# Kernel tuning notes

Measured on AMD Instinct MI355X. Metric: run time of the kernel, lower is better.

## Reference

```python
import jax, jax.numpy as jnp
import numpy as np

SINKHORN_ITERS = 10


def _optimal_transport(attn, phi, iters):
    # attn: [N,H,W,W], phi: scalar dustbin score
    bs, h, w, _ = attn.shape
    marginal = jnp.concatenate([jnp.ones((w,), attn.dtype), jnp.array([float(w)], attn.dtype)]) / (2.0 * w)
    log_mu = jnp.log(marginal)  # [W+1], broadcasts over [N,H,W+1]
    log_nu = log_mu
    # augment with dustbin row/col filled with phi -> [N,H,W+1,W+1]
    sim = jnp.concatenate([attn, jnp.broadcast_to(phi, (bs, h, w, 1))], axis=-1)
    sim = jnp.concatenate([sim, jnp.broadcast_to(phi, (bs, h, 1, w + 1))], axis=-2)

    def body(i, uv):
        u, v = uv
        v = log_nu - jax.nn.logsumexp(sim + u[..., :, None], axis=2)
        u = log_mu - jax.nn.logsumexp(sim + v[..., None, :], axis=3)
        return (u, v)

    u0 = jnp.zeros((bs, h, w + 1), attn.dtype)
    u, v = jax.lax.fori_loop(0, iters, body, (u0, u0))
    attn_ot = sim + u[..., :, None] + v[..., None, :]
    return jnp.exp(attn_ot + jnp.log(2.0 * w))


def _compute_low_res_disp(pos_shift, attn, occ_mask=None):
    # attn: [N,H,W,W] (dustbins removed); pos_shift: [W,W]
    w = attn.shape[-1]
    high_response = jnp.argmax(attn, axis=-1)  # [N,H,W]
    response_range = jnp.stack([high_response - 1, high_response, high_response + 1], axis=-1)  # [N,H,W,3]
    attn_pad = jnp.pad(attn, ((0, 0), (0, 0), (0, 0), (1, 1)))
    attn_rw = jnp.take_along_axis(attn_pad, response_range + 1, axis=-1)  # [N,H,W,3]
    norm = attn_rw.sum(-1, keepdims=True)
    norm = jnp.where(norm < 0.1, 1.0, norm)  # occ_mask is None branch
    attn_rw = attn_rw / norm
    pos_pad = jnp.pad(pos_shift, ((0, 0), (1, 1)))  # [W,W+2]
    pos_pad = jnp.broadcast_to(pos_pad[None, None], attn_pad.shape)
    pos_rw = jnp.take_along_axis(pos_pad, response_range + 1, axis=-1)
    disp = (attn_rw * pos_rw).sum(-1)  # [N,H,W]
    return disp, norm


def setup_inputs() -> dict:
    key = jax.random.key(0)
    k1, _ = jax.random.split(key)
    N, H, W = 4, 120, 256
    attn_weight = jax.random.normal(k1, (N, H, W, W), dtype=jnp.float32)
    phi = jnp.zeros((1,), dtype=jnp.float32)
    return {"attn_weight": attn_weight, "phi": phi}


def reference(attn_weight, phi):
    w = attn_weight.shape[2]
    attn_ot = _optimal_transport(attn_weight, phi[0], SINKHORN_ITERS)  # [N,H,W+1,W+1]
    # relative position shift, clamped at 0
    pos = jnp.arange(w, dtype=attn_weight.dtype)
    pos_shift = jnp.maximum(pos[:, None] - pos[None, :], 0.0)  # [W,W]
    disp_pred_low_res, matched_attn = _compute_low_res_disp(pos_shift, attn_ot[..., :-1, :-1], None)
    occ_pred = 1.0 - matched_attn.squeeze(-1)  # [N,H,W]
    return disp_pred_low_res, occ_pred
```

## Files before the change

### kernel.cpp

```cpp
#include <hip/hip_runtime.h>
#include <cstdint>

namespace {

constexpr int W = 256;
constexpr int ITERS = 10;
constexpr int PSTR = 260;

__device__ __forceinline__ float dpp_add_xor1(float x) {
  int y = __builtin_amdgcn_mov_dpp(__float_as_int(x), 0xB1, 0xF, 0xF, true);
  return x + __int_as_float(y);
}
__device__ __forceinline__ float dpp_add_xor2(float x) {
  int y = __builtin_amdgcn_mov_dpp(__float_as_int(x), 0x4E, 0xF, 0xF, true);
  return x + __int_as_float(y);
}
template <int PAT>
__device__ __forceinline__ float swz_add(float x) {
  return x + __int_as_float(__builtin_amdgcn_ds_swizzle(__float_as_int(x), PAT));
}
__device__ __forceinline__ float allred32(float x) {
  x = dpp_add_xor1(x);
  x = dpp_add_xor2(x);
  x = swz_add<0x101F>(x);
  x = swz_add<0x201F>(x);
  x = swz_add<0x401F>(x);
  return x;
}
__device__ __forceinline__ float rcpf(float x) {
  float r;
  asm("v_rcp_f32 %0, %1" : "=v"(r) : "v"(x));
  return r;
}

__global__ __launch_bounds__(1024)
void sinkhorn_disp_kernel(
    const float* __restrict__ attn,
    const float* __restrict__ phi_p,
    float* __restrict__ out,
    int nh)
{
  __shared__ __align__(16) float E_lds[1024 * 32];
  __shared__ __align__(16) float fpart[16][PSTR];
  __shared__ __align__(16) float ev_l[W];
  __shared__ __align__(16) float seup[32];
  __shared__ float evW_s;

  const int tid = threadIdx.x;
  const int tc  = tid & 31;
  const int tr  = tid >> 5;
  const int bid = blockIdx.x;
  const int sw  = tid & 7;
  float* myE = &E_lds[tid * 32];
  #define RDCH(c) (*(const float4*)&myE[4 * ((c) ^ sw)])

  const float ephi  = __int_as_float(
      __builtin_amdgcn_readfirstlane(__float_as_int(__expf(phi_p[0]))));
  const float inv2w = 1.0f / (2.0f * W);

  const int ch0 = 4 * ((2 * tc) ^ ((tc >> 2) & 7));

  float Er[5][8];
  {
    const float* src = attn + (size_t)bid * (W * W) + (size_t)(tr * 8) * W + tc * 8;
    #pragma unroll
    for (int a = 0; a < 5; ++a) {
      float4 x0 = *(const float4*)(src + a * W);
      float4 x1 = *(const float4*)(src + a * W + 4);
      Er[a][0] = __expf(x0.x); Er[a][1] = __expf(x0.y);
      Er[a][2] = __expf(x0.z); Er[a][3] = __expf(x0.w);
      Er[a][4] = __expf(x1.x); Er[a][5] = __expf(x1.y);
      Er[a][6] = __expf(x1.z); Er[a][7] = __expf(x1.w);
    }
    #pragma unroll
    for (int r = 0; r < 3; ++r) {
      float4 x0 = *(const float4*)(src + (5 + r) * W);
      float4 x1 = *(const float4*)(src + (5 + r) * W + 4);
      *(float4*)&myE[4 * ((2 + 2 * r) ^ sw)] =
          make_float4(__expf(x0.x), __expf(x0.y), __expf(x0.z), __expf(x0.w));
      *(float4*)&myE[4 * ((3 + 2 * r) ^ sw)] =
          make_float4(__expf(x1.x), __expf(x1.y), __expf(x1.z), __expf(x1.w));
    }
  }

  float eul[8];
  #pragma unroll
  for (int a = 0; a < 8; ++a) eul[a] = 1.0f;
  float euW = 1.0f;

  for (int it = 0; it < ITERS; ++it) {
    if (it >= 2 && it <= 5 && bid + 256 < nh) {
      const float* pf = attn + (size_t)(bid + 256) * (W * W)
                      + ((size_t)(it - 2) * 1024 + tid) * 16;
      float x = *pf;
      asm volatile("" :: "v"(x));
    }
    {
      float cp[8];
      #pragma unroll
      for (int b = 0; b < 8; ++b) cp[b] = 0.0f;
      #pragma unroll
      for (int a = 0; a < 5; ++a) {
        #pragma unroll
        for (int b = 0; b < 8; ++b)
          cp[b] = __builtin_fmaf(Er[a][b], eul[a], cp[b]);
      }
      #pragma unroll
      for (int r = 0; r < 3; ++r) {
        float4 e0 = RDCH(2 + 2 * r), e1 = RDCH(3 + 2 * r);
        float ua = eul[5 + r];
        cp[0] = __builtin_fmaf(e0.x, ua, cp[0]);
        cp[1] = __builtin_fmaf(e0.y, ua, cp[1]);
        cp[2] = __builtin_fmaf(e0.z, ua, cp[2]);
        cp[3] = __builtin_fmaf(e0.w, ua, cp[3]);
        cp[4] = __builtin_fmaf(e1.x, ua, cp[4]);
        cp[5] = __builtin_fmaf(e1.y, ua, cp[5]);
        cp[6] = __builtin_fmaf(e1.z, ua, cp[6]);
        cp[7] = __builtin_fmaf(e1.w, ua, cp[7]);
      }
      #pragma unroll
      for (int b = 0; b < 8; ++b) cp[b] += __shfl_xor(cp[b], 32, 64);
      if (!(tr & 1)) {
        *(float4*)&fpart[tr >> 1][ch0    ] = make_float4(cp[0], cp[1], cp[2], cp[3]);
        *(float4*)&fpart[tr >> 1][ch0 ^ 4] = make_float4(cp[4], cp[5], cp[6], cp[7]);
      }
      if (tc == 0)
        seup[tr] = ((eul[0] + eul[1]) + (eul[2] + eul[3]))
                 + ((eul[4] + eul[5]) + (eul[6] + eul[7]));
    }
    __syncthreads();
    if (tid < 2 * W) {
      const int j  = tid >> 1;
      const int fj = ((((j >> 2) ^ ((j >> 5) & 7)) << 2) | (j & 3));
      const int g0 = (tid & 1) * 8;
      float s = 0.0f;
      #pragma unroll
      for (int g = 0; g < 8; ++g) s += fpart[g0 + g][fj];
      s = dpp_add_xor1(s);
      if (!(tid & 1)) ev_l[fj] = inv2w * rcpf(s + ephi * euW);
    } else if ((tid >> 6) == 8) {
      float s = allred32(seup[tid & 31]);
      if (tid == 512) evW_s = 0.5f * rcpf(ephi * (s + euW));
    }
    __syncthreads();
    {
      const float evW = evW_s;
      float4 v0 = *(const float4*)&ev_l[ch0];
      float4 v1 = *(const float4*)&ev_l[ch0 ^ 4];
      float vl[8] = {v0.x, v0.y, v0.z, v0.w, v1.x, v1.y, v1.z, v1.w};
      float rp[8];
      #pragma unroll
      for (int a = 0; a < 5; ++a) {
        float s = 0.0f;
        #pragma unroll
        for (int b = 0; b < 8; ++b)
          s = __builtin_fmaf(Er[a][b], vl[b], s);
        rp[a] = s;
      }
      #pragma unroll
      for (int r = 0; r < 3; ++r) {
        float4 e0 = RDCH(2 + 2 * r), e1 = RDCH(3 + 2 * r);
        rp[5 + r] = e0.x * vl[0] + e0.y * vl[1] + e0.z * vl[2] + e0.w * vl[3]
                  + e1.x * vl[4] + e1.y * vl[5] + e1.z * vl[6] + e1.w * vl[7];
      }
      float sev = ((vl[0] + vl[1]) + (vl[2] + vl[3]))
                + ((vl[4] + vl[5]) + (vl[6] + vl[7]));
      #pragma unroll
      for (int a = 0; a < 8; ++a) rp[a] = allred32(rp[a]);
      sev = allred32(sev);
      const float eAdd = ephi * evW;
      #pragma unroll
      for (int a = 0; a < 8; ++a) eul[a] = inv2w * rcpf(rp[a] + eAdd);
      euW = 0.5f * rcpf(ephi * (sev + evW));
    }
  }

  float vl[8];
  {
    float4 v0 = *(const float4*)&ev_l[ch0];
    float4 v1 = *(const float4*)&ev_l[ch0 ^ 4];
    vl[0] = v0.x; vl[1] = v0.y; vl[2] = v0.z; vl[3] = v0.w;
    vl[4] = v1.x; vl[5] = v1.y; vl[6] = v1.z; vl[7] = v1.w;
  }
  float res_disp = 0.0f, res_occ = 0.0f;
  #pragma unroll
  for (int a = 0; a < 8; ++a) {
    float v[8];
    if (a < 5) {
      #pragma unroll
      for (int b = 0; b < 8; ++b) v[b] = Er[a < 5 ? a : 0][b] * vl[b];
    } else {
      float4 e0 = RDCH(2 + 2 * (a - 5)), e1 = RDCH(3 + 2 * (a - 5));
      v[0] = e0.x * vl[0]; v[1] = e0.y * vl[1];
      v[2] = e0.z * vl[2]; v[3] = e0.w * vl[3];
      v[4] = e1.x * vl[4]; v[5] = e1.y * vl[5];
      v[6] = e1.z * vl[6]; v[7] = e1.w * vl[7];
    }
    float m = v[0]; int mj = tc * 8;
    #pragma unroll
    for (int b = 1; b < 8; ++b) {
      if (v[b] > m) { m = v[b]; mj = tc * 8 + b; }
    }
    unsigned long long best =
        (((unsigned long long)__float_as_uint(m)) << 32) |
        (unsigned)(65535 - mj);
    #pragma unroll
    for (int off = 16; off > 0; off >>= 1) {
      unsigned long long o = __shfl_xor(best, off, 32);
      if (o > best) best = o;
    }
    const int jm = 65535 - (int)(best & 0xffffffffull);
    const int i  = tr * 8 + a;
    const float us = eul[a] * (2.0f * W);
    float num = 0.0f, den = 0.0f;
    #pragma unroll
    for (int b = 0; b < 8; ++b) {
      int j = tc * 8 + b;
      if (j >= jm - 1 && j <= jm + 1) {
        float w = v[b] * us;
        den += w;
        num += w * fmaxf((float)(i - j), 0.0f);
      }
    }
    den = allred32(den);
    num = allred32(num);
    if (tc == a) {
      float norm = (den < 0.1f) ? 1.0f : den;
      res_disp = num / norm;
      res_occ  = 1.0f - norm;
    }
  }
  if (tc < 8) {
    const int i = tr * 8 + tc;
    out[(size_t)bid * W + i] = res_disp;
    out[(size_t)nh * W + (size_t)bid * W + i] = res_occ;
  }
  #undef RDCH
}

}

extern "C" void kernel_launch(void* const* d_in, const int* in_sizes, int n_in,
                              void* d_out, int out_size, void* d_ws, size_t ws_size,
                              hipStream_t stream) {
  (void)n_in; (void)d_ws; (void)ws_size; (void)out_size;
  const float* attn = (const float*)d_in[0];
  const float* phi  = (const float*)d_in[1];
  float* out = (float*)d_out;
  const int nh = in_sizes[0] / (W * W);
  sinkhorn_disp_kernel<<<dim3(nh), dim3(1024), 0, stream>>>(attn, phi, out, nh);
}
```

Baseline: 235.8 us.

## Keep whole exp tile in registers with 512-thread blocks, drop LDS spill

Changes the block from 1024 threads holding 8 rows each (3 of them in LDS) to 512 threads holding 16 rows each entirely in registers (128 floats per thread). LDS traffic for the E matrix goes away, the partial-sum buffer is halved, and every thread computes the dustbin scalar redundantly instead of one wave reducing it. Launch bounds allow two blocks per CU. The risk is heavy register pressure: at 128+ VGPRs for E alone, occupancy may be limited or registers may spill, and the prefetch of the next tile now runs on more iterations.

```diff
diff --git a/kernel.cpp b/kernel.cpp
--- a/kernel.cpp
+++ b/kernel.cpp
@@ -33,65 +33,55 @@
   return r;
 }
 
-__global__ __launch_bounds__(1024)
+__global__ __launch_bounds__(512, 2)
 void sinkhorn_disp_kernel(
     const float* __restrict__ attn,
     const float* __restrict__ phi_p,
     float* __restrict__ out,
     int nh)
 {
-  __shared__ __align__(16) float E_lds[1024 * 32];
-  __shared__ __align__(16) float fpart[16][PSTR];
+  __shared__ __align__(16) float fpart[8][PSTR];
   __shared__ __align__(16) float ev_l[W];
-  __shared__ __align__(16) float seup[32];
-  __shared__ float evW_s;
-
-  const int tid = threadIdx.x;
-  const int tc  = tid & 31;
-  const int tr  = tid >> 5;
-  const int bid = blockIdx.x;
-  const int sw  = tid & 7;
-  float* myE = &E_lds[tid * 32];
-  #define RDCH(c) (*(const float4*)&myE[4 * ((c) ^ sw)])
-
-  const float ephi  = __int_as_float(
+  __shared__ __align__(16) float seup[16];
+
+  const int tid  = threadIdx.x;
+  const int lane = tid & 63;
+  const int wid  = tid >> 6;
+  const int cg   = lane & 31;
+  const int rg   = 2 * wid + (lane >> 5);
+  const int bid  = blockIdx.x;
+
+  const int ch0 = 4 * ((2 * cg) ^ ((cg >> 2) & 7));
+
+  const float ephi = __int_as_float(
       __builtin_amdgcn_readfirstlane(__float_as_int(__expf(phi_p[0]))));
   const float inv2w = 1.0f / (2.0f * W);
 
-  const int ch0 = 4 * ((2 * tc) ^ ((tc >> 2) & 7));
-
-  float Er[5][8];
+  float Er[16][8];
   {
-    const float* src = attn + (size_t)bid * (W * W) + (size_t)(tr * 8) * W + tc * 8;
-    #pragma unroll
-    for (int a = 0; a < 5; ++a) {
-      float4 x0 = *(const float4*)(src + a * W);
-      float4 x1 = *(const float4*)(src + a * W + 4);
-      Er[a][0] = __expf(x0.x); Er[a][1] = __expf(x0.y);
-      Er[a][2] = __expf(x0.z); Er[a][3] = __expf(x0.w);
-      Er[a][4] = __expf(x1.x); Er[a][5] = __expf(x1.y);
-      Er[a][6] = __expf(x1.z); Er[a][7] = __expf(x1.w);
-    }
-    #pragma unroll
-    for (int r = 0; r < 3; ++r) {
-      float4 x0 = *(const float4*)(src + (5 + r) * W);
-      float4 x1 = *(const float4*)(src + (5 + r) * W + 4);
-      *(float4*)&myE[4 * ((2 + 2 * r) ^ sw)] =
-          make_float4(__expf(x0.x), __expf(x0.y), __expf(x0.z), __expf(x0.w));
-      *(float4*)&myE[4 * ((3 + 2 * r) ^ sw)] =
-          make_float4(__expf(x1.x), __expf(x1.y), __expf(x1.z), __expf(x1.w));
-    }
-  }
-
-  float eul[8];
+    const float* src = attn + (size_t)bid * (W * W)
+                     + (size_t)(rg * 16) * W + cg * 8;
+    #pragma unroll
+    for (int r = 0; r < 16; ++r) {
+      float4 x0 = *(const float4*)(src + r * W);
+      float4 x1 = *(const float4*)(src + r * W + 4);
+      Er[r][0] = __expf(x0.x); Er[r][1] = __expf(x0.y);
+      Er[r][2] = __expf(x0.z); Er[r][3] = __expf(x0.w);
+      Er[r][4] = __expf(x1.x); Er[r][5] = __expf(x1.y);
+      Er[r][6] = __expf(x1.z); Er[r][7] = __expf(x1.w);
+    }
+  }
+
+  float eul[16];
   #pragma unroll
-  for (int a = 0; a < 8; ++a) eul[a] = 1.0f;
-  float euW = 1.0f;
+  for (int r = 0; r < 16; ++r) eul[r] = 1.0f;
+  float euW  = 1.0f;
+  float evWk = 0.0f;
 
   for (int it = 0; it < ITERS; ++it) {
-    if (it >= 2 && it <= 5 && bid + 256 < nh) {
+    if (it >= 2 && bid + 256 < nh) {
       const float* pf = attn + (size_t)(bid + 256) * (W * W)
-                      + ((size_t)(it - 2) * 1024 + tid) * 16;
+                      + ((size_t)(it - 2) * 512 + tid) * 16;
       float x = *pf;
       asm volatile("" :: "v"(x));
     }
@@ -100,78 +90,68 @@
       #pragma unroll
       for (int b = 0; b < 8; ++b) cp[b] = 0.0f;
       #pragma unroll
-      for (int a = 0; a < 5; ++a) {
+      for (int r = 0; r < 16; ++r) {
+        float u = eul[r];
         #pragma unroll
         for (int b = 0; b < 8; ++b)
-          cp[b] = __builtin_fmaf(Er[a][b], eul[a], cp[b]);
-      }
-      #pragma unroll
-      for (int r = 0; r < 3; ++r) {
-        float4 e0 = RDCH(2 + 2 * r), e1 = RDCH(3 + 2 * r);
-        float ua = eul[5 + r];
-        cp[0] = __builtin_fmaf(e0.x, ua, cp[0]);
-        cp[1] = __builtin_fmaf(e0.y, ua, cp[1]);
-        cp[2] = __builtin_fmaf(e0.z, ua, cp[2]);
-        cp[3] = __builtin_fmaf(e0.w, ua, cp[3]);
-        cp[4] = __builtin_fmaf(e1.x, ua, cp[4]);
-        cp[5] = __builtin_fmaf(e1.y, ua, cp[5]);
-        cp[6] = __builtin_fmaf(e1.z, ua, cp[6]);
-        cp[7] = __builtin_fmaf(e1.w, ua, cp[7]);
+          cp[b] = __builtin_fmaf(Er[r][b], u, cp[b]);
       }
       #pragma unroll
       for (int b = 0; b < 8; ++b) cp[b] += __shfl_xor(cp[b], 32, 64);
-      if (!(tr & 1)) {
-        *(float4*)&fpart[tr >> 1][ch0    ] = make_float4(cp[0], cp[1], cp[2], cp[3]);
-        *(float4*)&fpart[tr >> 1][ch0 ^ 4] = make_float4(cp[4], cp[5], cp[6], cp[7]);
-      }
-      if (tc == 0)
-        seup[tr] = ((eul[0] + eul[1]) + (eul[2] + eul[3]))
-                 + ((eul[4] + eul[5]) + (eul[6] + eul[7]));
+      if (lane < 32) {
+        *(float4*)&fpart[wid][ch0    ] = make_float4(cp[0], cp[1], cp[2], cp[3]);
+        *(float4*)&fpart[wid][ch0 ^ 4] = make_float4(cp[4], cp[5], cp[6], cp[7]);
+      }
+      if ((lane & 31) == 0) {
+        float s = (((eul[0] + eul[1]) + (eul[2] + eul[3]))
+                 + ((eul[4] + eul[5]) + (eul[6] + eul[7])))
+                + (((eul[8] + eul[9]) + (eul[10] + eul[11]))
+                 + ((eul[12] + eul[13]) + (eul[14] + eul[15])));
+        seup[rg] = s;
+      }
     }
     __syncthreads();
-    if (tid < 2 * W) {
+    {
       const int j  = tid >> 1;
       const int fj = ((((j >> 2) ^ ((j >> 5) & 7)) << 2) | (j & 3));
-      const int g0 = (tid & 1) * 8;
-      float s = 0.0f;
-      #pragma unroll
-      for (int g = 0; g < 8; ++g) s += fpart[g0 + g][fj];
+      const int g0 = (tid & 1) * 4;
+      float s = (fpart[g0][fj] + fpart[g0 + 1][fj])
+              + (fpart[g0 + 2][fj] + fpart[g0 + 3][fj]);
       s = dpp_add_xor1(s);
       if (!(tid & 1)) ev_l[fj] = inv2w * rcpf(s + ephi * euW);
-    } else if ((tid >> 6) == 8) {
-      float s = allred32(seup[tid & 31]);
-      if (tid == 512) evW_s = 0.5f * rcpf(ephi * (s + euW));
+      float4 s0 = *(const float4*)&seup[0];
+      float4 s1 = *(const float4*)&seup[4];
+      float4 s2 = *(const float4*)&seup[8];
+      float4 s3 = *(const float4*)&seup[12];
+      float Seu = ((((s0.x + s0.y) + (s0.z + s0.w))
+                  + ((s1.x + s1.y) + (s1.z + s1.w)))
+                 + (((s2.x + s2.y) + (s2.z + s2.w))
+                  + ((s3.x + s3.y) + (s3.z + s3.w))));
+      evWk = 0.5f * rcpf(ephi * (Seu + euW));
     }
     __syncthreads();
     {
-      const float evW = evW_s;
       float4 v0 = *(const float4*)&ev_l[ch0];
       float4 v1 = *(const float4*)&ev_l[ch0 ^ 4];
       float vl[8] = {v0.x, v0.y, v0.z, v0.w, v1.x, v1.y, v1.z, v1.w};
-      float rp[8];
-      #pragma unroll
-      for (int a = 0; a < 5; ++a) {
+      float rp[16];
+      #pragma unroll
+      for (int r = 0; r < 16; ++r) {
         float s = 0.0f;
         #pragma unroll
         for (int b = 0; b < 8; ++b)
-          s = __builtin_fmaf(Er[a][b], vl[b], s);
-        rp[a] = s;
-      }
-      #pragma unroll
-      for (int r = 0; r < 3; ++r) {
-        float4 e0 = RDCH(2 + 2 * r), e1 = RDCH(3 + 2 * r);
-        rp[5 + r] = e0.x * vl[0] + e0.y * vl[1] + e0.z * vl[2] + e0.w * vl[3]
-                  + e1.x * vl[4] + e1.y * vl[5] + e1.z * vl[6] + e1.w * vl[7];
+          s = __builtin_fmaf(Er[r][b], vl[b], s);
+        rp[r] = s;
       }
       float sev = ((vl[0] + vl[1]) + (vl[2] + vl[3]))
                 + ((vl[4] + vl[5]) + (vl[6] + vl[7]));
       #pragma unroll
-      for (int a = 0; a < 8; ++a) rp[a] = allred32(rp[a]);
+      for (int r = 0; r < 16; ++r) rp[r] = allred32(rp[r]);
       sev = allred32(sev);
-      const float eAdd = ephi * evW;
-      #pragma unroll
-      for (int a = 0; a < 8; ++a) eul[a] = inv2w * rcpf(rp[a] + eAdd);
-      euW = 0.5f * rcpf(ephi * (sev + evW));
+      const float eAdd = ephi * evWk;
+      #pragma unroll
+      for (int r = 0; r < 16; ++r) eul[r] = inv2w * rcpf(rp[r] + eAdd);
+      euW = 0.5f * rcpf(ephi * (sev + evWk));
     }
   }
 
@@ -184,22 +164,14 @@
   }
   float res_disp = 0.0f, res_occ = 0.0f;
   #pragma unroll
-  for (int a = 0; a < 8; ++a) {
+  for (int r = 0; r < 16; ++r) {
     float v[8];
-    if (a < 5) {
-      #pragma unroll
-      for (int b = 0; b < 8; ++b) v[b] = Er[a < 5 ? a : 0][b] * vl[b];
-    } else {
-      float4 e0 = RDCH(2 + 2 * (a - 5)), e1 = RDCH(3 + 2 * (a - 5));
-      v[0] = e0.x * vl[0]; v[1] = e0.y * vl[1];
-      v[2] = e0.z * vl[2]; v[3] = e0.w * vl[3];
-      v[4] = e1.x * vl[4]; v[5] = e1.y * vl[5];
-      v[6] = e1.z * vl[6]; v[7] = e1.w * vl[7];
-    }
-    float m = v[0]; int mj = tc * 8;
+    #pragma unroll
+    for (int b = 0; b < 8; ++b) v[b] = Er[r][b] * vl[b];
+    float m = v[0]; int mj = cg * 8;
     #pragma unroll
     for (int b = 1; b < 8; ++b) {
-      if (v[b] > m) { m = v[b]; mj = tc * 8 + b; }
+      if (v[b] > m) { m = v[b]; mj = cg * 8 + b; }
     }
     unsigned long long best =
         (((unsigned long long)__float_as_uint(m)) << 32) |
@@ -210,32 +182,31 @@
       if (o > best) best = o;
     }
     const int jm = 65535 - (int)(best & 0xffffffffull);
-    const int i  = tr * 8 + a;
-    const float us = eul[a] * (2.0f * W);
+    const int i  = rg * 16 + r;
+    const float us = eul[r] * (2.0f * W);
     float num = 0.0f, den = 0.0f;
     #pragma unroll
     for (int b = 0; b < 8; ++b) {
-      int j = tc * 8 + b;
+      int j = cg * 8 + b;
       if (j >= jm - 1 && j <= jm + 1) {
-        float w = v[b] * us;
-        den += w;
-        num += w * fmaxf((float)(i - j), 0.0f);
+        float wv = v[b] * us;
+        den += wv;
+        num += wv * fmaxf((float)(i - j), 0.0f);
       }
     }
     den = allred32(den);
     num = allred32(num);
-    if (tc == a) {
+    if (cg == r) {
       float norm = (den < 0.1f) ? 1.0f : den;
       res_disp = num / norm;
       res_occ  = 1.0f - norm;
     }
   }
-  if (tc < 8) {
-    const int i = tr * 8 + tc;
+  if (cg < 16) {
+    const int i = rg * 16 + cg;
     out[(size_t)bid * W + i] = res_disp;
     out[(size_t)nh * W + (size_t)bid * W + i] = res_occ;
   }
-  #undef RDCH
 }
 
 }
@@ -248,5 +219,5 @@
   const float* phi  = (const float*)d_in[1];
   float* out = (float*)d_out;
   const int nh = in_sizes[0] / (W * W);
-  sinkhorn_disp_kernel<<<dim3(nh), dim3(1024), 0, stream>>>(attn, phi, out, nh);
-}
+  sinkhorn_disp_kernel<<<dim3(nh), dim3(512), 0, stream>>>(attn, phi, out, nh);
+}
```

Result: no change. 235.4 us (-0.2%).
